# Kernel optimization log

Measured on AMD Instinct MI355X. Metric: run time of the kernel, lower is better.

The kernel has to match this reference:

```python
import jax, jax.numpy as jnp
import numpy as np
from jax import lax

NUM_PROPAGATIONS = 20
N_NODES = 100000
N_EDGES = 3200000
F_IN = 512
HIDDEN = 64
N_CLASSES = 64


def setup_inputs() -> dict:
    key = jax.random.key(0)
    ks = jax.random.split(key, 8)
    return {
        "node_features": jax.random.normal(ks[0], (N_NODES, F_IN), dtype=jnp.float32),
        "edge_weights": jax.random.uniform(ks[1], (N_EDGES,), dtype=jnp.float32),
        "W1": jax.random.normal(ks[2], (F_IN, HIDDEN), dtype=jnp.float32) * (1.0 / np.sqrt(F_IN)),
        "b1": jnp.zeros((HIDDEN,), dtype=jnp.float32),
        "W2": jax.random.normal(ks[3], (HIDDEN, N_CLASSES), dtype=jnp.float32) * (1.0 / np.sqrt(HIDDEN)),
        "b2": jnp.zeros((N_CLASSES,), dtype=jnp.float32),
        "Wg": jax.random.normal(ks[4], (N_CLASSES, 1), dtype=jnp.float32) * (1.0 / np.sqrt(N_CLASSES)),
        "bg": jnp.zeros((1,), dtype=jnp.float32),
        "senders": jax.random.randint(ks[5], (N_EDGES,), 0, N_NODES, dtype=jnp.int32),
        "receivers": jax.random.randint(ks[6], (N_EDGES,), 0, N_NODES, dtype=jnp.int32),
    }


def reference(node_features, edge_weights, W1, b1, W2, b2, Wg, bg, senders, receivers):
    n = node_features.shape[0]

    def spmm(x):  # sparse A @ x via gather + segment_sum, [n, c] -> [n, c]
        return jax.ops.segment_sum(edge_weights[:, None] * x[senders], receivers, num_segments=n)

    # MLP head (training=False -> dropout is identity)
    h = jax.nn.relu(node_features @ W1 + b1)          # [n, hidden]
    logits = h @ W2 + b2                              # [n, c]

    def step(carry, _):
        nxt = spmm(carry)
        return nxt, nxt

    _, hops = lax.scan(step, logits, None, length=NUM_PROPAGATIONS)  # [K, n, c]
    stack = jnp.concatenate([logits[:, None, :], jnp.transpose(hops, (1, 0, 2))], axis=1)  # [n, K+1, c]

    # GatedSum: sigmoid(Linear(1)) per hop, weighted sum over hops
    scale = jax.nn.sigmoid(jnp.squeeze(stack @ Wg + bg, axis=-1))    # [n, K+1]
    return jnp.einsum('nkl,nk->nl', stack, scale)                    # [n, c]
```

## Files before the change

### kernel.cpp

```cpp
#include <hip/hip_runtime.h>
#include <math.h>


#define F_IN 512
#define C 64

__device__ inline float h2f(ushort u) {
  _Float16 h; __builtin_memcpy(&h, &u, 2); return (float)h;
}
__device__ inline ushort f2h(float f) {
  _Float16 h = (_Float16)f; ushort u; __builtin_memcpy(&u, &h, 2); return u;
}

__global__ __launch_bounds__(256) void gemm1_relu(
    const float* __restrict__ A, const float* __restrict__ W1,
    const float* __restrict__ b1, float* __restrict__ H, int M)
{
  __shared__ __align__(16) float As[16][68];
  __shared__ __align__(16) float Bs[16][64];
  int t = threadIdx.x;
  int tx = t & 15, ty = t >> 4;
  int m0 = blockIdx.x * 64;
  int lm = t >> 2, lk = (t & 3) << 2;
  const float* Arow = A + (size_t)(m0 + lm) * F_IN;
  bool aok = (m0 + lm) < M;
  float acc[4][4] = {};

  for (int k0 = 0; k0 < F_IN; k0 += 16) {
    float4 av = make_float4(0.f, 0.f, 0.f, 0.f);
    if (aok) av = *(const float4*)(Arow + k0 + lk);
    float bv[4];
#pragma unroll
    for (int i = 0; i < 4; ++i)
      bv[i] = W1[(size_t)(k0 + (t >> 6) + (i << 2)) * C + (t & 63)];
    __syncthreads();
    As[lk + 0][lm] = av.x; As[lk + 1][lm] = av.y;
    As[lk + 2][lm] = av.z; As[lk + 3][lm] = av.w;
#pragma unroll
    for (int i = 0; i < 4; ++i)
      Bs[(t >> 6) + (i << 2)][t & 63] = bv[i];
    __syncthreads();
#pragma unroll
    for (int kk = 0; kk < 16; ++kk) {
      float4 a = *(const float4*)&As[kk][ty << 2];
      float4 b = *(const float4*)&Bs[kk][tx << 2];
      acc[0][0] += a.x * b.x; acc[0][1] += a.x * b.y; acc[0][2] += a.x * b.z; acc[0][3] += a.x * b.w;
      acc[1][0] += a.y * b.x; acc[1][1] += a.y * b.y; acc[1][2] += a.y * b.z; acc[1][3] += a.y * b.w;
      acc[2][0] += a.z * b.x; acc[2][1] += a.z * b.y; acc[2][2] += a.z * b.z; acc[2][3] += a.z * b.w;
      acc[3][0] += a.w * b.x; acc[3][1] += a.w * b.y; acc[3][2] += a.w * b.z; acc[3][3] += a.w * b.w;
    }
    __syncthreads();
  }
  float4 bb = *(const float4*)&b1[tx << 2];
#pragma unroll
  for (int i = 0; i < 4; ++i) {
    int row = m0 + (ty << 2) + i;
    if (row < M) {
      float4 r;
      r.x = fmaxf(acc[i][0] + bb.x, 0.f);
      r.y = fmaxf(acc[i][1] + bb.y, 0.f);
      r.z = fmaxf(acc[i][2] + bb.z, 0.f);
      r.w = fmaxf(acc[i][3] + bb.w, 0.f);
      *(float4*)&H[(size_t)row * C + (tx << 2)] = r;
    }
  }
}

__global__ __launch_bounds__(256) void gemm2_gate(
    const float* __restrict__ h, const float* __restrict__ W2,
    const float* __restrict__ b2, const float* __restrict__ Wg,
    const float* __restrict__ bgp, ushort* __restrict__ x0,
    float* __restrict__ out, int n, int write_out)
{
  __shared__ float W2s[C * C];
  int t = threadIdx.x;
  for (int i = t; i < C * C; i += blockDim.x) W2s[i] = W2[i];
  __syncthreads();
  int lane = t & 63, wid = t >> 6;
  int wave = blockIdx.x * (blockDim.x >> 6) + wid;
  int nw = gridDim.x * (blockDim.x >> 6);
  float wg = Wg[lane], bgv = bgp[0], b2v = b2[lane];
  for (int node = wave; node < n; node += nw) {
    float hv = h[(size_t)node * C + lane];
    float acc = b2v;
#pragma unroll
    for (int k = 0; k < C; ++k) {
      float hk = __shfl(hv, k, 64);
      acc += hk * W2s[k * C + lane];
    }
    size_t o = (size_t)node * C + lane;
    x0[o] = f2h(acc);
    if (write_out) {
      float p = acc * wg;
#pragma unroll
      for (int off = 32; off > 0; off >>= 1) p += __shfl_xor(p, off, 64);
      float g = 1.f / (1.f + expf(-(p + bgv)));
      out[o] = g * acc;
    }
  }
}

__global__ void zero_int(int* __restrict__ p, int n) {
  int i = blockIdx.x * blockDim.x + threadIdx.x;
  if (i < n) p[i] = 0;
}

__global__ void hist_recv(const int* __restrict__ recv, int* __restrict__ cnt, int E) {
  int i = blockIdx.x * blockDim.x + threadIdx.x;
  if (i < E) atomicAdd(&cnt[recv[i]], 1);
}

__global__ __launch_bounds__(1024) void scan_counts(
    int* __restrict__ cnt_cursor, int* __restrict__ row_start, int n)
{
  __shared__ int wsum[16];
  int t = threadIdx.x, lane = t & 63, wid = t >> 6;
  int carry = 0;
  for (int base = 0; base < n; base += 1024) {
    int idx = base + t;
    int v = (idx < n) ? cnt_cursor[idx] : 0;
    int incl = v;
#pragma unroll
    for (int off = 1; off < 64; off <<= 1) {
      int u = __shfl_up(incl, off, 64);
      if (lane >= off) incl += u;
    }
    if (lane == 63) wsum[wid] = incl;
    __syncthreads();
    if (t < 16) {
      int ws = wsum[t];
#pragma unroll
      for (int off = 1; off < 16; off <<= 1) {
        int u = __shfl_up(ws, off, 16);
        if ((t & 15) >= off) ws += u;
      }
      wsum[t] = ws;
    }
    __syncthreads();
    int woff = (wid > 0) ? wsum[wid - 1] : 0;
    int total = wsum[15];
    int excl = carry + woff + (incl - v);
    if (idx < n) { row_start[idx] = excl; cnt_cursor[idx] = excl; }
    carry += total;
    __syncthreads();
  }
  if (t == 0) row_start[n] = carry;
}

__global__ void scatter_edges(
    const int* __restrict__ send, const int* __restrict__ recv,
    const float* __restrict__ ew, int* __restrict__ cursor,
    int2* __restrict__ csr, int E)
{
  int i = blockIdx.x * blockDim.x + threadIdx.x;
  if (i < E) {
    int r = recv[i];
    int p = atomicAdd(&cursor[r], 1);
    csr[p] = make_int2(send[i], __float_as_int(ew[i]));
  }
}

__global__ __launch_bounds__(256) void spmm_pair(
    const ushort* __restrict__ x, const int* __restrict__ row_start,
    const int2* __restrict__ csr, ushort* __restrict__ x_next, int n)
{
  int t = threadIdx.x;
  int lane = t & 63, wid = t >> 6;
  int half = lane >> 5;
  int ch2 = (lane & 31) << 1;
  int wave = blockIdx.x * 4 + wid;
  int nw = gridDim.x * 4;

  for (int node = wave; node < n; node += nw) {
    int beg = row_start[node], end = row_start[node + 1];
    float ax0 = 0.f, ay0 = 0.f, ax1 = 0.f, ay1 = 0.f;
    float ax2 = 0.f, ay2 = 0.f, ax3 = 0.f, ay3 = 0.f;
    for (int base = beg; base < end; base += 64) {
      int2 ev = make_int2(0, 0);
      if (base + lane < end) ev = csr[base + lane];
      int cnt = end - base; if (cnt > 64) cnt = 64;
      int j = 0;
      for (; j + 8 <= cnt; j += 8) {
        int i0 = j + 0 + half, i1 = j + 2 + half;
        int i2 = j + 4 + half, i3 = j + 6 + half;
        int   s0 = __shfl(ev.x, i0, 64), s1 = __shfl(ev.x, i1, 64);
        int   s2 = __shfl(ev.x, i2, 64), s3 = __shfl(ev.x, i3, 64);
        float w0 = __int_as_float(__shfl(ev.y, i0, 64));
        float w1 = __int_as_float(__shfl(ev.y, i1, 64));
        float w2 = __int_as_float(__shfl(ev.y, i2, 64));
        float w3 = __int_as_float(__shfl(ev.y, i3, 64));
        ushort2 u0 = *(const ushort2*)&x[(unsigned)(s0 * C) + ch2];
        ushort2 u1 = *(const ushort2*)&x[(unsigned)(s1 * C) + ch2];
        ushort2 u2 = *(const ushort2*)&x[(unsigned)(s2 * C) + ch2];
        ushort2 u3 = *(const ushort2*)&x[(unsigned)(s3 * C) + ch2];
        ax0 += w0 * h2f(u0.x); ay0 += w0 * h2f(u0.y);
        ax1 += w1 * h2f(u1.x); ay1 += w1 * h2f(u1.y);
        ax2 += w2 * h2f(u2.x); ay2 += w2 * h2f(u2.y);
        ax3 += w3 * h2f(u3.x); ay3 += w3 * h2f(u3.y);
      }
      for (; j < cnt; j += 2) {
        int i0 = j + half;
        int s0 = __shfl(ev.x, i0, 64);
        float w0 = __int_as_float(__shfl(ev.y, i0, 64));
        ushort2 u0 = *(const ushort2*)&x[(unsigned)(s0 * C) + ch2];
        ax0 += w0 * h2f(u0.x); ay0 += w0 * h2f(u0.y);
      }
    }
    float sx = (ax0 + ax1) + (ax2 + ax3);
    float sy = (ay0 + ay1) + (ay2 + ay3);
    sx += __shfl_xor(sx, 32, 64);
    sy += __shfl_xor(sy, 32, 64);
    if (half == 0) {
      ushort2 uv;
      uv.x = f2h(sx * 0.0625f);
      uv.y = f2h(sy * 0.0625f);
      *(ushort2*)&x_next[(size_t)node * C + ch2] = uv;
    }
  }
}

__global__ __launch_bounds__(256) void gate_sum(
    const ushort* __restrict__ slots, const float* __restrict__ Wg,
    const float* __restrict__ bgp, float* __restrict__ out,
    int n, int K1, size_t slotStride)
{
  int t = threadIdx.x;
  int lane = t & 63, wid = t >> 6;
  int wave = blockIdx.x * 4 + wid;
  int nw = gridDim.x * 4;
  float wg = Wg[lane], bgv = bgp[0];
  for (int node = wave; node < n; node += nw) {
    float acc = 0.f;
    float scale = 1.f;
    size_t o = (size_t)node * C + lane;
    for (int k = 0; k < K1; ++k) {
      float v = h2f(slots[(size_t)k * slotStride + o]);
      float p = v * wg;
#pragma unroll
      for (int off = 32; off > 0; off >>= 1) p += __shfl_xor(p, off, 64);
      float g = 1.f / (1.f + expf(-(p * scale + bgv)));
      acc += g * (v * scale);
      scale *= 16.f;
    }
    out[o] = acc;
  }
}

__global__ __launch_bounds__(256) void spmm_gate(
    const ushort* __restrict__ x, const int* __restrict__ row_start,
    const int2* __restrict__ csr, const float* __restrict__ Wg,
    const float* __restrict__ bgp, ushort* __restrict__ x_next,
    float* __restrict__ out, int n, float s_in)
{
  int t = threadIdx.x;
  int lane = t & 63, wid = t >> 6;
  int wave = blockIdx.x * (blockDim.x >> 6) + wid;
  int nw = gridDim.x * (blockDim.x >> 6);
  float wg = Wg[lane], bgv = bgp[0];

  for (int node = wave; node < n; node += nw) {
    int beg = row_start[node], end = row_start[node + 1];
    float a0 = 0.f, a1 = 0.f, a2 = 0.f, a3 = 0.f;
    for (int base = beg; base < end; base += 64) {
      int2 ev = make_int2(0, 0);
      if (base + lane < end) ev = csr[base + lane];
      int cnt = end - base; if (cnt > 64) cnt = 64;
      int j = 0;
      for (; j + 4 <= cnt; j += 4) {
        int   s0 = __shfl(ev.x, j + 0, 64), s1 = __shfl(ev.x, j + 1, 64);
        int   s2 = __shfl(ev.x, j + 2, 64), s3 = __shfl(ev.x, j + 3, 64);
        float w0 = __int_as_float(__shfl(ev.y, j + 0, 64));
        float w1 = __int_as_float(__shfl(ev.y, j + 1, 64));
        float w2 = __int_as_float(__shfl(ev.y, j + 2, 64));
        float w3 = __int_as_float(__shfl(ev.y, j + 3, 64));
        a0 += w0 * h2f(x[(unsigned)(s0 * C) + lane]);
        a1 += w1 * h2f(x[(unsigned)(s1 * C) + lane]);
        a2 += w2 * h2f(x[(unsigned)(s2 * C) + lane]);
        a3 += w3 * h2f(x[(unsigned)(s3 * C) + lane]);
      }
      for (; j < cnt; ++j) {
        int sj = __shfl(ev.x, j, 64);
        float wj = __int_as_float(__shfl(ev.y, j, 64));
        a0 += wj * h2f(x[(unsigned)(sj * C) + lane]);
      }
    }
    float acc = (a0 + a1) + (a2 + a3);
    float p = acc * wg;
#pragma unroll
    for (int off = 32; off > 0; off >>= 1) p += __shfl_xor(p, off, 64);
    float g = 1.f / (1.f + expf(-(p * s_in + bgv)));
    size_t o = (size_t)node * C + lane;
    x_next[o] = f2h(acc * 0.0625f);
    out[o] += g * (acc * s_in);
  }
}

extern "C" void kernel_launch(void* const* d_in, const int* in_sizes, int n_in,
                              void* d_out, int out_size, void* d_ws, size_t ws_size,
                              hipStream_t stream) {
  const float* nf   = (const float*)d_in[0];
  const float* ew   = (const float*)d_in[1];
  const float* W1   = (const float*)d_in[2];
  const float* b1   = (const float*)d_in[3];
  const float* W2   = (const float*)d_in[4];
  const float* b2   = (const float*)d_in[5];
  const float* Wg   = (const float*)d_in[6];
  const float* bg   = (const float*)d_in[7];
  const int* send   = (const int*)d_in[8];
  const int* recv   = (const int*)d_in[9];
  float* out = (float*)d_out;

  int n = in_sizes[0] / F_IN;
  int E = in_sizes[1];
  const int K = 20;

  size_t slotElems = (size_t)n * C;
  size_t need = slotElems * 4
              + (size_t)(K + 1) * slotElems * 2
              + (size_t)E * 8
              + (size_t)(2 * n + 1) * 4;

  if (ws_size >= need) {
    float*  hbuf = (float*)d_ws;
    ushort* slots = (ushort*)(hbuf + slotElems);
    int2*   csr  = (int2*)(slots + (size_t)(K + 1) * slotElems);
    int* row_start = (int*)(csr + E);
    int* cursor    = row_start + (n + 1);

    gemm1_relu<<<(n + 63) / 64, 256, 0, stream>>>(nf, W1, b1, hbuf, n);
    gemm2_gate<<<(n + 3) / 4, 256, 0, stream>>>(hbuf, W2, b2, Wg, bg,
                                                slots, out, n, 0);

    zero_int<<<(n + 255) / 256, 256, 0, stream>>>(cursor, n);
    hist_recv<<<(E + 255) / 256, 256, 0, stream>>>(recv, cursor, E);
    scan_counts<<<1, 1024, 0, stream>>>(cursor, row_start, n);
    scatter_edges<<<(E + 255) / 256, 256, 0, stream>>>(send, recv, ew, cursor,
                                                       csr, E);

    for (int k = 0; k < K; ++k) {
      spmm_pair<<<(n + 3) / 4, 256, 0, stream>>>(
          slots + (size_t)k * slotElems, row_start, csr,
          slots + (size_t)(k + 1) * slotElems, n);
    }
    gate_sum<<<(n + 3) / 4, 256, 0, stream>>>(slots, Wg, bg, out, n, K + 1,
                                              slotElems);
  } else {
    float*  hbuf = (float*)d_ws;
    ushort* xA   = (ushort*)(hbuf + slotElems);
    ushort* xB   = xA + slotElems;
    int2*   csr  = (int2*)(xB + slotElems);
    int* row_start = (int*)(csr + E);
    int* cursor    = row_start + (n + 1);

    gemm1_relu<<<(n + 63) / 64, 256, 0, stream>>>(nf, W1, b1, hbuf, n);
    gemm2_gate<<<(n + 3) / 4, 256, 0, stream>>>(hbuf, W2, b2, Wg, bg,
                                                xA, out, n, 1);

    zero_int<<<(n + 255) / 256, 256, 0, stream>>>(cursor, n);
    hist_recv<<<(E + 255) / 256, 256, 0, stream>>>(recv, cursor, E);
    scan_counts<<<1, 1024, 0, stream>>>(cursor, row_start, n);
    scatter_edges<<<(E + 255) / 256, 256, 0, stream>>>(send, recv, ew, cursor,
                                                       csr, E);

    ushort* xin = xA;
    ushort* xout = xB;
    for (int k = 0; k < K; ++k) {
      float s_in = ldexpf(1.0f, 4 * k);
      spmm_gate<<<(n + 3) / 4, 256, 0, stream>>>(xin, row_start, csr, Wg, bg,
                                                 xout, out, n, s_in);
      ushort* tmp = xin; xin = xout; xout = tmp;
    }
  }
}
```

Before: 2.258 ms.

## Build CSR via two-pass bucketed binning instead of random atomic scatter

Replaces the single random-scatter CSR build, one global atomic and one scattered 8-byte write per edge, with two passes. The first bins edges into 512-node buckets, staging them in shared memory so writes to an intermediate buffer (reusing the unused hop slots) are coalesced. The second scatters within each bucket using shared-memory atomics, so writes stay in a local region. This trades an extra pass over the edge data for better write locality and fewer global atomics, and it relies on packing the sender index into 17 bits.

```diff
diff --git a/kernel.cpp b/kernel.cpp
--- a/kernel.cpp
+++ b/kernel.cpp
@@ -4,6 +4,10 @@
 
 #define F_IN 512
 #define C 64
+#define BSHIFT 9
+#define BMASK ((1 << BSHIFT) - 1)
+#define CHUNK 4096
+#define EPT 16
 
 __device__ inline float h2f(ushort u) {
   _Float16 h; __builtin_memcpy(&h, &u, 2); return (float)h;
@@ -145,6 +149,105 @@
     __syncthreads();
   }
   if (t == 0) row_start[n] = carry;
+}
+
+__global__ void init_gcur(const int* __restrict__ row_start,
+                          int* __restrict__ gcur, int NB) {
+  int t = blockIdx.x * blockDim.x + threadIdx.x;
+  if (t < NB) gcur[t] = row_start[t << BSHIFT];
+}
+
+__global__ __launch_bounds__(256) void bin_edges(
+    const int* __restrict__ send, const int* __restrict__ recv,
+    const float* __restrict__ ew, int* __restrict__ gcur,
+    int2* __restrict__ ibuf, int E, int NB)
+{
+  __shared__ int cnt[256];
+  __shared__ int offs[256];
+  __shared__ int gb[256];
+  __shared__ int wsum[4];
+  __shared__ int2 stage[CHUNK];
+  __shared__ unsigned char sb[CHUNK];
+
+  int t = threadIdx.x;
+  int base = blockIdx.x * CHUNK;
+  int valid = E - base; if (valid > CHUNK) valid = CHUNK;
+
+  cnt[t] = 0;
+  __syncthreads();
+
+  int2 pk[EPT];
+  int bk[EPT];
+#pragma unroll
+  for (int r = 0; r < EPT; ++r) {
+    int e = base + r * 256 + t;
+    bk[r] = -1;
+    if (e < E) {
+      int rc = recv[e];
+      int b = rc >> BSHIFT;
+      pk[r] = make_int2(send[e] | ((rc & BMASK) << 17), __float_as_int(ew[e]));
+      bk[r] = b;
+      atomicAdd(&cnt[b], 1);
+    }
+  }
+  __syncthreads();
+
+  {
+    int lane = t & 63, wid = t >> 6;
+    int v = cnt[t];
+    int incl = v;
+#pragma unroll
+    for (int off = 1; off < 64; off <<= 1) {
+      int u = __shfl_up(incl, off, 64);
+      if (lane >= off) incl += u;
+    }
+    if (lane == 63) wsum[wid] = incl;
+    __syncthreads();
+    int w0 = wsum[0], w1 = wsum[1], w2 = wsum[2];
+    int woff = (wid == 0) ? 0 : (wid == 1) ? w0 : (wid == 2) ? w0 + w1
+                                                             : w0 + w1 + w2;
+    int excl = woff + incl - v;
+    offs[t] = excl;
+    if (t < NB && v > 0) gb[t] = atomicAdd(&gcur[t], v);
+    cnt[t] = excl;
+  }
+  __syncthreads();
+
+#pragma unroll
+  for (int r = 0; r < EPT; ++r) {
+    if (bk[r] >= 0) {
+      int slot = atomicAdd(&cnt[bk[r]], 1);
+      stage[slot] = pk[r];
+      sb[slot] = (unsigned char)bk[r];
+    }
+  }
+  __syncthreads();
+
+  for (int s = t; s < valid; s += 256) {
+    int b = sb[s];
+    ibuf[gb[b] + (s - offs[b])] = stage[s];
+  }
+}
+
+__global__ __launch_bounds__(256) void scatter_bucket(
+    const int2* __restrict__ ibuf, const int* __restrict__ row_start,
+    int2* __restrict__ csr, int n)
+{
+  __shared__ int cur[1 << BSHIFT];
+  int b = blockIdx.x;
+  int nodeBase = b << BSHIFT;
+  int nNodes = n - nodeBase; if (nNodes > (1 << BSHIFT)) nNodes = 1 << BSHIFT;
+  int t = threadIdx.x;
+  for (int i = t; i < nNodes; i += 256) cur[i] = row_start[nodeBase + i];
+  __syncthreads();
+  int beg = row_start[nodeBase];
+  int end = row_start[nodeBase + nNodes];
+  for (int i = beg + t; i < end; i += 256) {
+    int2 e = ibuf[i];
+    int rl = (e.x >> 17) & BMASK;
+    int p = atomicAdd(&cur[rl], 1);
+    csr[p] = make_int2(e.x & 0x1FFFF, e.y);
+  }
 }
 
 __global__ void scatter_edges(
@@ -313,19 +416,22 @@
   int n = in_sizes[0] / F_IN;
   int E = in_sizes[1];
   const int K = 20;
+  int NB = (n + BMASK) >> BSHIFT;
 
   size_t slotElems = (size_t)n * C;
   size_t need = slotElems * 4
               + (size_t)(K + 1) * slotElems * 2
               + (size_t)E * 8
-              + (size_t)(2 * n + 1) * 4;
-
-  if (ws_size >= need) {
+              + (size_t)(2 * n + 1 + NB) * 4;
+
+  if (ws_size >= need && E * 2 <= (int)(K * slotElems / 4)) {
     float*  hbuf = (float*)d_ws;
     ushort* slots = (ushort*)(hbuf + slotElems);
     int2*   csr  = (int2*)(slots + (size_t)(K + 1) * slotElems);
     int* row_start = (int*)(csr + E);
     int* cursor    = row_start + (n + 1);
+    int* gcur      = cursor + n;
+    int2* ibuf     = (int2*)(slots + slotElems);
 
     gemm1_relu<<<(n + 63) / 64, 256, 0, stream>>>(nf, W1, b1, hbuf, n);
     gemm2_gate<<<(n + 3) / 4, 256, 0, stream>>>(hbuf, W2, b2, Wg, bg,
@@ -334,8 +440,10 @@
     zero_int<<<(n + 255) / 256, 256, 0, stream>>>(cursor, n);
     hist_recv<<<(E + 255) / 256, 256, 0, stream>>>(recv, cursor, E);
     scan_counts<<<1, 1024, 0, stream>>>(cursor, row_start, n);
-    scatter_edges<<<(E + 255) / 256, 256, 0, stream>>>(send, recv, ew, cursor,
-                                                       csr, E);
+    init_gcur<<<(NB + 255) / 256, 256, 0, stream>>>(row_start, gcur, NB);
+    bin_edges<<<(E + CHUNK - 1) / CHUNK, 256, 0, stream>>>(send, recv, ew,
+                                                           gcur, ibuf, E, NB);
+    scatter_bucket<<<NB, 256, 0, stream>>>(ibuf, row_start, csr, n);
 
     for (int k = 0; k < K; ++k) {
       spmm_pair<<<(n + 3) / 4, 256, 0, stream>>>(
```

Result: faster. 2.050 ms (-9.2%).
